# Performance work log

Measured on AMD Instinct MI355X. Metric: run time of the kernel, lower is better.

## Reference

```python
import jax, jax.numpy as jnp
import numpy as np

B, T, D, U = 32, 512, 1024, 1024
EPS = 1e-08


def setup_inputs() -> dict:
    key = jax.random.key(0)
    k1, k2, k3 = jax.random.split(key, 3)
    # scale weights for numerical sanity (glorot/orthogonal-ish magnitudes)
    kernel = jax.random.normal(k1, (D, 4 * U), dtype=jnp.float32) * (1.0 / np.sqrt(D))
    recurrent_kernel = jax.random.normal(k2, (U, 4 * U), dtype=jnp.float32) * (1.0 / np.sqrt(U))
    bias = jnp.zeros((4 * U,), dtype=jnp.float32)
    x = jax.random.normal(k3, (B, T, D), dtype=jnp.float32)
    return {"x": x, "kernel": kernel, "recurrent_kernel": recurrent_kernel, "bias": bias}


def reference(x, kernel, recurrent_kernel, bias):
    """sLSTM (xLSTM Sec 2.2) with sigmoid forget gate + log/exp/max stabilization,
    scanned over the time axis. Returns h of shape (B, T, U)."""
    U_ = bias.shape[0] // 4
    Bsz = x.shape[0]
    # precompute input projections for all timesteps: (T, B, 4U)
    x_proj = jnp.einsum('btd,dg->tbg', x, kernel) + bias

    def step(carry, xp_t):
        h, c, n, m = carry
        proj = xp_t + h @ recurrent_kernel          # (B, 4U)
        i_p, f_p, o_p, z_p = jnp.split(proj, 4, axis=-1)
        log_f = jnp.log(jax.nn.sigmoid(f_p) + EPS)
        m_t = jnp.maximum(m + log_f, i_p)
        i_t = jnp.exp(i_p - m_t)
        f_t = jnp.exp(m + log_f - m_t)
        o_t = jax.nn.sigmoid(o_p)
        z_t = jnp.tanh(z_p)
        c_t = f_t * c + i_t * z_t
        n_t = f_t * n + i_t
        h_t = o_t * (c_t / (n_t + EPS))
        return (h_t, c_t, n_t, m_t), h_t

    zeros = jnp.zeros((Bsz, U_), dtype=x.dtype)
    init = (zeros, zeros, zeros, zeros)
    _, hs = jax.lax.scan(step, init, x_proj)        # hs: (T, B, U)
    return jnp.transpose(hs, (1, 0, 2))             # (B, T, U)
```

## Files before the change

### kernel.cpp

```cpp
#include <hip/hip_runtime.h>

typedef unsigned short u16;
typedef short short8 __attribute__((ext_vector_type(8)));
typedef float f32x4 __attribute__((ext_vector_type(4)));
typedef unsigned int u32x4 __attribute__((ext_vector_type(4)));
typedef unsigned int u32x2 __attribute__((ext_vector_type(2)));
typedef unsigned short u16x4 __attribute__((ext_vector_type(4)));

#define Bsz 32
#define Tsz 512
#define Dsz 1024
#define Usz 1024
#define Gsz 4096

static __device__ __forceinline__ u16 f2bf(float f) {
    unsigned int u = __float_as_uint(f);
    unsigned int lsb = (u >> 16) & 1u;
    u += 0x7fffu + lsb;
    return (u16)(u >> 16);
}
static __device__ __forceinline__ float bf2f(u16 b) {
    return __uint_as_float(((unsigned int)b) << 16);
}


__global__ __launch_bounds__(256) void pack_a(const float* __restrict__ x, u16* __restrict__ Af) {
    size_t tid = (size_t)blockIdx.x * 256 + threadIdx.x;
    int L = (int)(tid & 63);
    size_t mtkb = tid >> 6;
    int kb = (int)(mtkb & 31);
    int mt = (int)(mtkb >> 5);
    int m  = mt * 16 + (L & 15);
    int d0 = kb * 32 + (L >> 4) * 8;
    const float* src = x + (size_t)m * Dsz + d0;
    short8 v;
#pragma unroll
    for (int j = 0; j < 8; ++j) v[j] = (short)f2bf(src[j]);
    *(short8*)(Af + tid * 8) = v;
}

__global__ __launch_bounds__(256) void pack_b(const float* __restrict__ W, u16* __restrict__ Bf) {
    size_t tid = (size_t)blockIdx.x * 256 + threadIdx.x;
    int L = (int)(tid & 63);
    size_t ntkb = tid >> 6;
    int kb = (int)(ntkb & 31);
    int nt = (int)(ntkb >> 5);
    int n  = nt * 16 + (L & 15);
    int k0 = kb * 32 + (L >> 4) * 8;
    short8 v;
#pragma unroll
    for (int j = 0; j < 8; ++j) v[j] = (short)f2bf(W[(size_t)(k0 + j) * Gsz + n]);
    *(short8*)(Bf + tid * 8) = v;
}

__global__ __launch_bounds__(256) void pack_r(const float* __restrict__ R, u16* __restrict__ Rp,
                                              unsigned* __restrict__ flags) {
    if (blockIdx.x < 2) flags[blockIdx.x * 256 + threadIdx.x] = 0;
    size_t tid = (size_t)blockIdx.x * 256 + threadIdx.x;
    int L = (int)(tid & 63);
    size_t bkkb = tid >> 6;
    int kb  = (int)(bkkb & 31);
    int blk = (int)(bkkb >> 5);
    int c = L & 15;
    int gate = c >> 2, du = c & 3;
    int g = gate * 1024 + blk * 4 + du;
    int k0 = kb * 32 + (L >> 4) * 8;
    short8 v;
#pragma unroll
    for (int j = 0; j < 8; ++j) v[j] = (short)f2bf(R[(size_t)(k0 + j) * Gsz + g]);
    *(short8*)(Rp + tid * 8) = v;
}

__global__ __launch_bounds__(256) void gemm1(const u16* __restrict__ Af, const u16* __restrict__ Bf,
                                             float* __restrict__ xpf, u16* __restrict__ xph, int xp32) {
    __shared__ u16 smem[16 * 512];
    int bm = blockIdx.x >> 5;
    int bn = blockIdx.x & 31;
    int tid = threadIdx.x;
    int w = tid >> 6, ln = tid & 63;
    int mw = w & 1, nw = w >> 1;

    f32x4 acc[4][4];
#pragma unroll
    for (int i = 0; i < 4; ++i)
#pragma unroll
        for (int j = 0; j < 4; ++j) acc[i][j] = (f32x4){0.f, 0.f, 0.f, 0.f};

    for (int kb = 0; kb < 32; ++kb) {
        short8 tmp[4];
#pragma unroll
        for (int c2 = 0; c2 < 4; ++c2) {
            int chunk = w * 4 + c2;
            const u16* src = (chunk < 8)
                ? Af + (((size_t)(bm * 8 + chunk) * 32 + kb) * 64 + ln) * 8
                : Bf + (((size_t)(bn * 8 + (chunk - 8)) * 32 + kb) * 64 + ln) * 8;
            tmp[c2] = *(const short8*)src;
        }
#pragma unroll
        for (int c2 = 0; c2 < 4; ++c2) {
            int chunk = w * 4 + c2;
            *(short8*)(smem + chunk * 512 + ln * 8) = tmp[c2];
        }
        __syncthreads();
        short8 av[4], bv[4];
#pragma unroll
        for (int i = 0; i < 4; ++i) av[i] = *(const short8*)(smem + (mw * 4 + i) * 512 + ln * 8);
#pragma unroll
        for (int j = 0; j < 4; ++j) bv[j] = *(const short8*)(smem + (8 + nw * 4 + j) * 512 + ln * 8);
#pragma unroll
        for (int i = 0; i < 4; ++i)
#pragma unroll
            for (int j = 0; j < 4; ++j)
                acc[i][j] = __builtin_amdgcn_mfma_f32_16x16x32_bf16(av[i], bv[j], acc[i][j], 0, 0, 0);
        __syncthreads();
    }

    int quad = ln >> 4, c15 = ln & 15;
#pragma unroll
    for (int i = 0; i < 4; ++i) {
        int mt_g = bm * 8 + mw * 4 + i;
#pragma unroll
        for (int j = 0; j < 4; ++j) {
            int g = (bn * 8 + nw * 4 + j) * 16 + c15;
            int p = ((g & 1023) >> 2) * 16 + (g & 3) * 4 + (g >> 10);
#pragma unroll
            for (int r = 0; r < 4; ++r) {
                int row = mt_g * 16 + quad * 4 + r;
                int bb = row >> 9, tt = row & 511;
                size_t o = ((size_t)tt * Bsz + bb) * Gsz + p;
                if (xp32) xpf[o] = acc[i][j][r];
                else      xph[o] = f2bf(acc[i][j][r]);
            }
        }
    }
}

__global__ __launch_bounds__(384) void scan_all(const float* __restrict__ xpf,
                                                const u16* __restrict__ xph, int xp32,
                                                const u16* __restrict__ Rp,
                                                const float* __restrict__ bias,
                                                u16* __restrict__ hbf, float* __restrict__ out,
                                                unsigned* __restrict__ flags) {
    __shared__ u16 lds_r[16384];
    __shared__ f32x4 partial[2][4][64];
    __shared__ float proj[16][17];

    int tid = threadIdx.x;
    int blk = blockIdx.x;
    int w = tid >> 6, ln = tid & 63, quad = ln >> 4, c15 = ln & 15;
    int bq = ln >> 2, du = ln & 3;
    int u_g = blk * 4 + du;

    unsigned* flags0 = flags;
    unsigned* flags1 = flags + 256;

    u16* h00 = hbf;
    u16* h01 = hbf + 16384;
    u16* h10 = hbf + 32768;
    u16* h11 = hbf + 49152;

    if (tid < 256) {
#pragma unroll
        for (int i = 0; i < 8; ++i)
            *(short8*)(lds_r + tid * 64 + i * 8) = *(const short8*)(Rp + (size_t)blk * 16384 + tid * 64 + i * 8);
        u32x4 z = (u32x4){0u, 0u, 0u, 0u};
#pragma unroll
        for (int i = 0; i < 8; ++i) {
            u16* p0 = h01 + tid * 64 + i * 8;
            u16* p1 = h11 + tid * 64 + i * 8;
            asm volatile("global_store_dwordx4 %0, %1, off sc0 sc1" :: "v"(p0), "v"(z) : "memory");
            asm volatile("global_store_dwordx4 %0, %1, off sc0 sc1" :: "v"(p1), "v"(z) : "memory");
        }
    }

    float bi0 = 0.f, bi1 = 0.f, bi2 = 0.f, bi3 = 0.f;
    float cs = 0.f, ns = 0.f, ms = 0.f;
    f32x4 xr4 = (f32x4){0.f, 0.f, 0.f, 0.f};
    u32x2 xr2 = (u32x2){0u, 0u};

    if (w >= 4) {
        int G = w - 4;
        bi0 = bias[u_g]; bi1 = bias[1024 + u_g]; bi2 = bias[2048 + u_g]; bi3 = bias[3072 + u_g];
        size_t o0 = (size_t)(G * 16 + bq) * Gsz + blk * 16 + du * 4;
        if (xp32) xr4 = *(const f32x4*)(xpf + o0);
        else      xr2 = *(const u32x2*)(xph + o0);
    }
    asm volatile("s_waitcnt vmcnt(0)" ::: "memory");
    __syncthreads();
    if (tid == 0) {
        unsigned one = 1;
        unsigned* f0 = flags0 + blk;
        unsigned* f1 = flags1 + blk;
        asm volatile("global_store_dword %0, %1, off sc0 sc1" :: "v"(f0), "v"(one) : "memory");
        asm volatile("global_store_dword %0, %1, off sc0 sc1" :: "v"(f1), "v"(one) : "memory");
    }

    auto phase = [&](int G, int t) {
        if (w < 4) {
            const unsigned* fp4 = (G ? flags1 : flags0) + ln * 4;
            unsigned tgt = (unsigned)(t + 1);
            u32x4 fv;
            do {
                asm volatile("global_load_dwordx4 %0, %1, off sc0 sc1\n\ts_waitcnt vmcnt(0)"
                             : "=v"(fv) : "v"(fp4) : "memory");
            } while (__any((int)(fv[0] < tgt || fv[1] < tgt || fv[2] < tgt || fv[3] < tgt)));

            const u16* hload = G ? ((t & 1) ? h10 : h11) : ((t & 1) ? h00 : h01);
            const u16* aBw = hload + (size_t)c15 * 1024 + w * 256 + quad * 8;
            short8 av[8];
#define LDH(i, OFF) asm volatile("global_load_dwordx4 %0, %1, off offset:" OFF " sc0 sc1" \
                                 : "=v"(av[i]) : "v"(aBw))
            LDH(0, "0");   LDH(1, "64");  LDH(2, "128"); LDH(3, "192");
            LDH(4, "256"); LDH(5, "320"); LDH(6, "384"); LDH(7, "448");
#undef LDH
            asm volatile("s_waitcnt vmcnt(0)" ::: "memory");
            __builtin_amdgcn_sched_barrier(0);

            f32x4 a0 = (f32x4){0.f, 0.f, 0.f, 0.f};
            f32x4 a1 = (f32x4){0.f, 0.f, 0.f, 0.f};
#pragma unroll
            for (int kk = 0; kk < 8; kk += 2) {
                short8 b0 = *(const short8*)(lds_r + ((w * 8 + kk) * 64 + ln) * 8);
                short8 b1 = *(const short8*)(lds_r + ((w * 8 + kk + 1) * 64 + ln) * 8);
                a0 = __builtin_amdgcn_mfma_f32_16x16x32_bf16(av[kk], b0, a0, 0, 0, 0);
                a1 = __builtin_amdgcn_mfma_f32_16x16x32_bf16(av[kk + 1], b1, a1, 0, 0, 0);
            }
            partial[G][w][ln] = a0 + a1;
        }
        __syncthreads();
        if (w == 4 + G) {
            f32x4 s = partial[G][0][ln];
            s += partial[G][1][ln];
            s += partial[G][2][ln];
            s += partial[G][3][ln];
#pragma unroll
            for (int r = 0; r < 4; ++r) proj[quad * 4 + r][c15] = s[r];
            asm volatile("s_waitcnt lgkmcnt(0)" ::: "memory");
            __builtin_amdgcn_sched_barrier(0);

            asm volatile("s_waitcnt vmcnt(0)" : "+v"(xr4), "+v"(xr2) :: "memory");
            __builtin_amdgcn_sched_barrier(0);
            float xv0, xv1, xv2, xv3;
            if (xp32) { xv0 = xr4[0]; xv1 = xr4[1]; xv2 = xr4[2]; xv3 = xr4[3]; }
            else {
                xv0 = bf2f((u16)(xr2[0] & 0xffffu)); xv1 = bf2f((u16)(xr2[0] >> 16));
                xv2 = bf2f((u16)(xr2[1] & 0xffffu)); xv3 = bf2f((u16)(xr2[1] >> 16));
            }

            float ip  = proj[bq][du]      + xv0 + bi0;
            float fp_ = proj[bq][4 + du]  + xv1 + bi1;
            float op_ = proj[bq][8 + du]  + xv2 + bi2;
            float zp  = proj[bq][12 + du] + xv3 + bi3;
            float sf = 1.f / (1.f + __expf(-fp_));
            float lf = __logf(sf + 1e-8f);
            float mn = fmaxf(ms + lf, ip);
            float it = __expf(ip - mn);
            float ft = __expf(ms + lf - mn);
            float ot = 1.f / (1.f + __expf(-op_));
            float zt = tanhf(zp);
            cs = ft * cs + it * zt;
            ns = ft * ns + it;
            ms = mn;
            float h = ot * (cs / (ns + 1e-8f));
            out[(size_t)(G * 16 + bq) * (Tsz * Usz) + (size_t)t * Usz + u_g] = h;
            u16* hstore = G ? ((t & 1) ? h11 : h10) : ((t & 1) ? h01 : h00);
            u16* hp = hstore + bq * 1024 + u_g;
            unsigned hv = (unsigned)f2bf(h);
            asm volatile("global_store_short %0, %1, off sc0 sc1" :: "v"(hp), "v"(hv) : "memory");
            asm volatile("s_waitcnt vmcnt(0)" ::: "memory");
            __builtin_amdgcn_sched_barrier(0);
            if (ln == 0) {
                unsigned* fm = (G ? flags1 : flags0) + blk;
                unsigned val = (unsigned)(t + 2);
                asm volatile("global_store_dword %0, %1, off sc0 sc1" :: "v"(fm), "v"(val) : "memory");
            }
            int tn = (t + 1 < Tsz) ? t + 1 : t;
            size_t o = ((size_t)tn * Bsz + (G * 16 + bq)) * Gsz + blk * 16 + du * 4;
            if (xp32) {
                const float* p = xpf + o;
                asm volatile("global_load_dwordx4 %0, %1, off" : "=v"(xr4) : "v"(p));
            } else {
                const u16* p = xph + o;
                asm volatile("global_load_dwordx2 %0, %1, off" : "=v"(xr2) : "v"(p));
            }
        }
    };

    for (int t = 0; t < Tsz; ++t) {
        phase(0, t);
        phase(1, t);
    }
}

extern "C" void kernel_launch(void* const* d_in, const int* in_sizes, int n_in,
                              void* d_out, int out_size, void* d_ws, size_t ws_size,
                              hipStream_t stream) {
    const float* x    = (const float*)d_in[0];
    const float* W    = (const float*)d_in[1];
    const float* R    = (const float*)d_in[2];
    const float* bias = (const float*)d_in[3];
    float* out = (float*)d_out;

    char* ws = (char*)d_ws;
    size_t off = 0;
    u16* Af = (u16*)(ws + off); off += (size_t)16384 * 1024 * 2;
    u16* Bf = (u16*)(ws + off); off += (size_t)1024 * 4096 * 2;
    u16* Rp = (u16*)(ws + off); off += (size_t)1024 * 4096 * 2;
    u16* hbf = (u16*)(ws + off); off += (size_t)1 << 20;
    unsigned* flags = (unsigned*)(ws + off); off += 4096;
    size_t xp_need32 = (size_t)16384 * 4096 * 4;
    int xp32 = (ws_size >= off + xp_need32) ? 1 : 0;
    float* xpf = (float*)(ws + off);
    u16*   xph = (u16*)(ws + off);

    pack_a<<<dim3(8192), dim3(256), 0, stream>>>(x, Af);
    pack_b<<<dim3(2048), dim3(256), 0, stream>>>(W, Bf);
    pack_r<<<dim3(2048), dim3(256), 0, stream>>>(R, Rp, flags);
    gemm1<<<dim3(4096), dim3(256), 0, stream>>>(Af, Bf, xpf, xph, xp32);

    void* args[] = { (void*)&xpf, (void*)&xph, (void*)&xp32, (void*)&Rp,
                     (void*)&bias, (void*)&hbf, (void*)&out, (void*)&flags };
    hipLaunchCooperativeKernel((const void*)scan_all, dim3(256), dim3(384), args, 0, stream);
}
```

Measured before the change: 2.615 ms.

## Specialize scan waves with LDS flag handoff instead of block barriers

Splits the persistent scan block into role-specialized waves: two poller waves spin on global flags and publish readiness through LDS, four MFMA waves keep their recurrent-weight slice in registers instead of LDS, and two gate waves consume double-buffered partials. Per-step __syncthreads are replaced by volatile LDS counters, so the two batch halves can pipeline independently. The block grows to 512 threads. This adds register pressure, spin-waiting on LDS, and a risk of memory-ordering bugs in the flag handoff.

Result: slower. 5.068 ms (+93.8%).

```diff
diff --git a/kernel.cpp b/kernel.cpp
--- a/kernel.cpp
+++ b/kernel.cpp
@@ -135,15 +135,16 @@
     }
 }
 
-__global__ __launch_bounds__(384) void scan_all(const float* __restrict__ xpf,
+__global__ __launch_bounds__(512) void scan_all(const float* __restrict__ xpf,
                                                 const u16* __restrict__ xph, int xp32,
                                                 const u16* __restrict__ Rp,
                                                 const float* __restrict__ bias,
                                                 u16* __restrict__ hbf, float* __restrict__ out,
                                                 unsigned* __restrict__ flags) {
-    __shared__ u16 lds_r[16384];
-    __shared__ f32x4 partial[2][4][64];
-    __shared__ float proj[16][17];
+    __shared__ f32x4 partial[2][2][4][64];
+    __shared__ float proj[2][16][17];
+    __shared__ int ready_sh[2];
+    __shared__ int done_sh[2][4];
 
     int tid = threadIdx.x;
     int blk = blockIdx.x;
@@ -159,10 +160,10 @@
     u16* h10 = hbf + 32768;
     u16* h11 = hbf + 49152;
 
+    if (tid == 0) { ready_sh[0] = 0; ready_sh[1] = 0; }
+    if (tid < 8) ((int*)done_sh)[tid] = 0;
+
     if (tid < 256) {
-#pragma unroll
-        for (int i = 0; i < 8; ++i)
-            *(short8*)(lds_r + tid * 64 + i * 8) = *(const short8*)(Rp + (size_t)blk * 16384 + tid * 64 + i * 8);
         u32x4 z = (u32x4){0u, 0u, 0u, 0u};
 #pragma unroll
         for (int i = 0; i < 8; ++i) {
@@ -174,11 +175,10 @@
     }
 
     float bi0 = 0.f, bi1 = 0.f, bi2 = 0.f, bi3 = 0.f;
-    float cs = 0.f, ns = 0.f, ms = 0.f;
     f32x4 xr4 = (f32x4){0.f, 0.f, 0.f, 0.f};
     u32x2 xr2 = (u32x2){0u, 0u};
 
-    if (w >= 4) {
+    if (w == 4 || w == 5) {
         int G = w - 4;
         bi0 = bias[u_g]; bi1 = bias[1024 + u_g]; bi2 = bias[2048 + u_g]; bi3 = bias[3072 + u_g];
         size_t o0 = (size_t)(G * 16 + bq) * Gsz + blk * 16 + du * 4;
@@ -186,6 +186,7 @@
         else      xr2 = *(const u32x2*)(xph + o0);
     }
     asm volatile("s_waitcnt vmcnt(0)" ::: "memory");
+    __builtin_amdgcn_sched_barrier(0);
     __syncthreads();
     if (tid == 0) {
         unsigned one = 1;
@@ -195,46 +196,61 @@
         asm volatile("global_store_dword %0, %1, off sc0 sc1" :: "v"(f1), "v"(one) : "memory");
     }
 
-    auto phase = [&](int G, int t) {
-        if (w < 4) {
-            const unsigned* fp4 = (G ? flags1 : flags0) + ln * 4;
-            unsigned tgt = (unsigned)(t + 1);
-            u32x4 fv;
-            do {
-                asm volatile("global_load_dwordx4 %0, %1, off sc0 sc1\n\ts_waitcnt vmcnt(0)"
-                             : "=v"(fv) : "v"(fp4) : "memory");
-            } while (__any((int)(fv[0] < tgt || fv[1] < tgt || fv[2] < tgt || fv[3] < tgt)));
-
-            const u16* hload = G ? ((t & 1) ? h10 : h11) : ((t & 1) ? h00 : h01);
-            const u16* aBw = hload + (size_t)c15 * 1024 + w * 256 + quad * 8;
-            short8 av[8];
+    if (w < 4) {
+        short8 rB[8];
+#pragma unroll
+        for (int kk = 0; kk < 8; ++kk)
+            rB[kk] = *(const short8*)(Rp + (size_t)blk * 16384 + (size_t)(((w * 8 + kk) * 64 + ln) * 8));
+
+        volatile int* rdy0 = &ready_sh[0];
+        volatile int* rdy1 = &ready_sh[1];
+
+        for (int t = 0; t < Tsz; ++t) {
+#pragma unroll
+            for (int G = 0; G < 2; ++G) {
+                volatile int* rdy = G ? rdy1 : rdy0;
+                while (*rdy < t + 1) { }
+                __builtin_amdgcn_sched_barrier(0);
+
+                const u16* hload = G ? ((t & 1) ? h10 : h11) : ((t & 1) ? h00 : h01);
+                const u16* aBw = hload + (size_t)c15 * 1024 + w * 256 + quad * 8;
+                short8 av[8];
 #define LDH(i, OFF) asm volatile("global_load_dwordx4 %0, %1, off offset:" OFF " sc0 sc1" \
                                  : "=v"(av[i]) : "v"(aBw))
-            LDH(0, "0");   LDH(1, "64");  LDH(2, "128"); LDH(3, "192");
-            LDH(4, "256"); LDH(5, "320"); LDH(6, "384"); LDH(7, "448");
+                LDH(0, "0");   LDH(1, "64");  LDH(2, "128"); LDH(3, "192");
+                LDH(4, "256"); LDH(5, "320"); LDH(6, "384"); LDH(7, "448");
 #undef LDH
-            asm volatile("s_waitcnt vmcnt(0)" ::: "memory");
-            __builtin_amdgcn_sched_barrier(0);
-
-            f32x4 a0 = (f32x4){0.f, 0.f, 0.f, 0.f};
-            f32x4 a1 = (f32x4){0.f, 0.f, 0.f, 0.f};
-#pragma unroll
-            for (int kk = 0; kk < 8; kk += 2) {
-                short8 b0 = *(const short8*)(lds_r + ((w * 8 + kk) * 64 + ln) * 8);
-                short8 b1 = *(const short8*)(lds_r + ((w * 8 + kk + 1) * 64 + ln) * 8);
-                a0 = __builtin_amdgcn_mfma_f32_16x16x32_bf16(av[kk], b0, a0, 0, 0, 0);
-                a1 = __builtin_amdgcn_mfma_f32_16x16x32_bf16(av[kk + 1], b1, a1, 0, 0, 0);
-            }
-            partial[G][w][ln] = a0 + a1;
-        }
-        __syncthreads();
-        if (w == 4 + G) {
-            f32x4 s = partial[G][0][ln];
-            s += partial[G][1][ln];
-            s += partial[G][2][ln];
-            s += partial[G][3][ln];
-#pragma unroll
-            for (int r = 0; r < 4; ++r) proj[quad * 4 + r][c15] = s[r];
+                asm volatile("s_waitcnt vmcnt(0)" ::: "memory");
+                __builtin_amdgcn_sched_barrier(0);
+
+                f32x4 a0 = (f32x4){0.f, 0.f, 0.f, 0.f};
+                f32x4 a1 = (f32x4){0.f, 0.f, 0.f, 0.f};
+#pragma unroll
+                for (int kk = 0; kk < 8; kk += 2) {
+                    a0 = __builtin_amdgcn_mfma_f32_16x16x32_bf16(av[kk],     rB[kk],     a0, 0, 0, 0);
+                    a1 = __builtin_amdgcn_mfma_f32_16x16x32_bf16(av[kk + 1], rB[kk + 1], a1, 0, 0, 0);
+                }
+                partial[G][t & 1][w][ln] = a0 + a1;
+                asm volatile("s_waitcnt lgkmcnt(0)" ::: "memory");
+                __builtin_amdgcn_sched_barrier(0);
+                if (ln == 0) *((volatile int*)&done_sh[G][w]) = t + 1;
+            }
+        }
+    } else if (w < 6) {
+        int G = w - 4;
+        float cs = 0.f, ns = 0.f, ms = 0.f;
+        volatile int* dp = &done_sh[G][ln & 3];
+
+        for (int t = 0; t < Tsz; ++t) {
+            while (__any(*dp < t + 1)) { }
+            __builtin_amdgcn_sched_barrier(0);
+
+            f32x4 s = partial[G][t & 1][0][ln];
+            s += partial[G][t & 1][1][ln];
+            s += partial[G][t & 1][2][ln];
+            s += partial[G][t & 1][3][ln];
+#pragma unroll
+            for (int r = 0; r < 4; ++r) proj[G][quad * 4 + r][c15] = s[r];
             asm volatile("s_waitcnt lgkmcnt(0)" ::: "memory");
             __builtin_amdgcn_sched_barrier(0);
 
@@ -247,10 +263,10 @@
                 xv2 = bf2f((u16)(xr2[1] & 0xffffu)); xv3 = bf2f((u16)(xr2[1] >> 16));
             }
 
-            float ip  = proj[bq][du]      + xv0 + bi0;
-            float fp_ = proj[bq][4 + du]  + xv1 + bi1;
-            float op_ = proj[bq][8 + du]  + xv2 + bi2;
-            float zp  = proj[bq][12 + du] + xv3 + bi3;
+            float ip  = proj[G][bq][du]      + xv0 + bi0;
+            float fp_ = proj[G][bq][4 + du]  + xv1 + bi1;
+            float op_ = proj[G][bq][8 + du]  + xv2 + bi2;
+            float zp  = proj[G][bq][12 + du] + xv3 + bi3;
             float sf = 1.f / (1.f + __expf(-fp_));
             float lf = __logf(sf + 1e-8f);
             float mn = fmaxf(ms + lf, ip);
@@ -284,11 +300,19 @@
                 asm volatile("global_load_dwordx2 %0, %1, off" : "=v"(xr2) : "v"(p));
             }
         }
-    };
-
-    for (int t = 0; t < Tsz; ++t) {
-        phase(0, t);
-        phase(1, t);
+    } else {
+        int G = w - 6;
+        const unsigned* fp4 = (G ? flags1 : flags0) + ln * 4;
+        for (int s = 1; s <= Tsz; ++s) {
+            unsigned tgt = (unsigned)s;
+            u32x4 fv;
+            do {
+                asm volatile("global_load_dwordx4 %0, %1, off sc0 sc1\n\ts_waitcnt vmcnt(0)"
+                             : "=v"(fv) : "v"(fp4) : "memory");
+            } while (__any((int)(fv[0] < tgt || fv[1] < tgt || fv[2] < tgt || fv[3] < tgt)));
+            __builtin_amdgcn_sched_barrier(0);
+            if (ln == 0) *((volatile int*)&ready_sh[G]) = s;
+        }
     }
 }
 
@@ -320,5 +344,5 @@
 
     void* args[] = { (void*)&xpf, (void*)&xph, (void*)&xp32, (void*)&Rp,
                      (void*)&bias, (void*)&hbf, (void*)&out, (void*)&flags };
-    hipLaunchCooperativeKernel((const void*)scan_all, dim3(256), dim3(384), args, 0, stream);
-}
+    hipLaunchCooperativeKernel((const void*)scan_all, dim3(256), dim3(512), args, 0, stream);
+}
```

## Replace per-block flag polling with NaN-sentinel validity check on h buffers

Applied to the files above, without the earlier changes.

Removes the separate flag array and its spin loop. Consumers now load h directly and retry until no element holds the NaN sentinel. The h state becomes a 4-slot ring per group: each step writes h into one slot and resets the slot two steps ahead to the sentinel. pack_r initialises the ring instead of zeroing flags. This cuts the flag-poll round trip from the critical path of every timestep, at the risk of a false match if a real bf16 h value is NaN or Inf, plus extra sentinel stores and per-element checks.

Measured after the change: 2.472 ms. 1.06x faster.

```diff
diff --git a/kernel.cpp b/kernel.cpp
--- a/kernel.cpp
+++ b/kernel.cpp
@@ -5,13 +5,14 @@
 typedef float f32x4 __attribute__((ext_vector_type(4)));
 typedef unsigned int u32x4 __attribute__((ext_vector_type(4)));
 typedef unsigned int u32x2 __attribute__((ext_vector_type(2)));
-typedef unsigned short u16x4 __attribute__((ext_vector_type(4)));
 
 #define Bsz 32
 #define Tsz 512
 #define Dsz 1024
 #define Usz 1024
 #define Gsz 4096
+
+#define SENTINEL 0x7FC0u
 
 static __device__ __forceinline__ u16 f2bf(float f) {
     unsigned int u = __float_as_uint(f);
@@ -54,9 +55,12 @@
 }
 
 __global__ __launch_bounds__(256) void pack_r(const float* __restrict__ R, u16* __restrict__ Rp,
-                                              unsigned* __restrict__ flags) {
-    if (blockIdx.x < 2) flags[blockIdx.x * 256 + threadIdx.x] = 0;
+                                              u16* __restrict__ hbf) {
     size_t tid = (size_t)blockIdx.x * 256 + threadIdx.x;
+    if (tid < 131072) {
+        int p = (int)((tid >> 14) & 3);
+        hbf[tid] = (p == 3) ? (u16)0 : (u16)SENTINEL;
+    }
     int L = (int)(tid & 63);
     size_t bkkb = tid >> 6;
     int kb  = (int)(bkkb & 31);
@@ -139,11 +143,10 @@
                                                 const u16* __restrict__ xph, int xp32,
                                                 const u16* __restrict__ Rp,
                                                 const float* __restrict__ bias,
-                                                u16* __restrict__ hbf, float* __restrict__ out,
-                                                unsigned* __restrict__ flags) {
+                                                u16* __restrict__ hbf, float* __restrict__ out) {
     __shared__ u16 lds_r[16384];
     __shared__ f32x4 partial[2][4][64];
-    __shared__ float proj[16][17];
+    __shared__ float proj[2][16][17];
 
     int tid = threadIdx.x;
     int blk = blockIdx.x;
@@ -151,26 +154,10 @@
     int bq = ln >> 2, du = ln & 3;
     int u_g = blk * 4 + du;
 
-    unsigned* flags0 = flags;
-    unsigned* flags1 = flags + 256;
-
-    u16* h00 = hbf;
-    u16* h01 = hbf + 16384;
-    u16* h10 = hbf + 32768;
-    u16* h11 = hbf + 49152;
-
     if (tid < 256) {
 #pragma unroll
         for (int i = 0; i < 8; ++i)
             *(short8*)(lds_r + tid * 64 + i * 8) = *(const short8*)(Rp + (size_t)blk * 16384 + tid * 64 + i * 8);
-        u32x4 z = (u32x4){0u, 0u, 0u, 0u};
-#pragma unroll
-        for (int i = 0; i < 8; ++i) {
-            u16* p0 = h01 + tid * 64 + i * 8;
-            u16* p1 = h11 + tid * 64 + i * 8;
-            asm volatile("global_store_dwordx4 %0, %1, off sc0 sc1" :: "v"(p0), "v"(z) : "memory");
-            asm volatile("global_store_dwordx4 %0, %1, off sc0 sc1" :: "v"(p1), "v"(z) : "memory");
-        }
     }
 
     float bi0 = 0.f, bi1 = 0.f, bi2 = 0.f, bi3 = 0.f;
@@ -185,35 +172,35 @@
         if (xp32) xr4 = *(const f32x4*)(xpf + o0);
         else      xr2 = *(const u32x2*)(xph + o0);
     }
-    asm volatile("s_waitcnt vmcnt(0)" ::: "memory");
     __syncthreads();
-    if (tid == 0) {
-        unsigned one = 1;
-        unsigned* f0 = flags0 + blk;
-        unsigned* f1 = flags1 + blk;
-        asm volatile("global_store_dword %0, %1, off sc0 sc1" :: "v"(f0), "v"(one) : "memory");
-        asm volatile("global_store_dword %0, %1, off sc0 sc1" :: "v"(f1), "v"(one) : "memory");
-    }
 
     auto phase = [&](int G, int t) {
         if (w < 4) {
-            const unsigned* fp4 = (G ? flags1 : flags0) + ln * 4;
-            unsigned tgt = (unsigned)(t + 1);
-            u32x4 fv;
-            do {
-                asm volatile("global_load_dwordx4 %0, %1, off sc0 sc1\n\ts_waitcnt vmcnt(0)"
-                             : "=v"(fv) : "v"(fp4) : "memory");
-            } while (__any((int)(fv[0] < tgt || fv[1] < tgt || fv[2] < tgt || fv[3] < tgt)));
-
-            const u16* hload = G ? ((t & 1) ? h10 : h11) : ((t & 1) ? h00 : h01);
-            const u16* aBw = hload + (size_t)c15 * 1024 + w * 256 + quad * 8;
+            const u16* hbase = hbf + ((size_t)(G * 4 + ((t + 3) & 3)) << 14)
+                                   + (size_t)c15 * 1024 + w * 256 + quad * 8;
             short8 av[8];
+            for (;;) {
 #define LDH(i, OFF) asm volatile("global_load_dwordx4 %0, %1, off offset:" OFF " sc0 sc1" \
-                                 : "=v"(av[i]) : "v"(aBw))
-            LDH(0, "0");   LDH(1, "64");  LDH(2, "128"); LDH(3, "192");
-            LDH(4, "256"); LDH(5, "320"); LDH(6, "384"); LDH(7, "448");
+                                 : "=v"(av[i]) : "v"(hbase))
+                LDH(0, "0");   LDH(1, "64");  LDH(2, "128"); LDH(3, "192");
+                LDH(4, "256"); LDH(5, "320"); LDH(6, "384"); LDH(7, "448");
 #undef LDH
-            asm volatile("s_waitcnt vmcnt(0)" ::: "memory");
+                asm volatile("s_waitcnt vmcnt(0)" ::: "memory");
+                __builtin_amdgcn_sched_barrier(0);
+                unsigned bad = 0;
+#pragma unroll
+                for (int i = 0; i < 8; ++i) {
+                    u32x4 xw = __builtin_bit_cast(u32x4, av[i]);
+#pragma unroll
+                    for (int k = 0; k < 4; ++k) {
+                        unsigned m = xw[k] & 0x7F807F80u;
+                        bad |= (unsigned)((m >> 16) == 0x7F80u);
+                        bad |= (unsigned)((m & 0xFFFFu) == 0x7F80u);
+                    }
+                }
+                if (!__any((int)bad)) break;
+                asm volatile("s_sleep 1" ::: "memory");
+            }
             __builtin_amdgcn_sched_barrier(0);
 
             f32x4 a0 = (f32x4){0.f, 0.f, 0.f, 0.f};
@@ -234,7 +221,7 @@
             s += partial[G][2][ln];
             s += partial[G][3][ln];
 #pragma unroll
-            for (int r = 0; r < 4; ++r) proj[quad * 4 + r][c15] = s[r];
+            for (int r = 0; r < 4; ++r) proj[G][quad * 4 + r][c15] = s[r];
             asm volatile("s_waitcnt lgkmcnt(0)" ::: "memory");
             __builtin_amdgcn_sched_barrier(0);
 
@@ -247,10 +234,10 @@
                 xv2 = bf2f((u16)(xr2[1] & 0xffffu)); xv3 = bf2f((u16)(xr2[1] >> 16));
             }
 
-            float ip  = proj[bq][du]      + xv0 + bi0;
-            float fp_ = proj[bq][4 + du]  + xv1 + bi1;
-            float op_ = proj[bq][8 + du]  + xv2 + bi2;
-            float zp  = proj[bq][12 + du] + xv3 + bi3;
+            float ip  = proj[G][bq][du]      + xv0 + bi0;
+            float fp_ = proj[G][bq][4 + du]  + xv1 + bi1;
+            float op_ = proj[G][bq][8 + du]  + xv2 + bi2;
+            float zp  = proj[G][bq][12 + du] + xv3 + bi3;
             float sf = 1.f / (1.f + __expf(-fp_));
             float lf = __logf(sf + 1e-8f);
             float mn = fmaxf(ms + lf, ip);
@@ -263,17 +250,17 @@
             ms = mn;
             float h = ot * (cs / (ns + 1e-8f));
             out[(size_t)(G * 16 + bq) * (Tsz * Usz) + (size_t)t * Usz + u_g] = h;
-            u16* hstore = G ? ((t & 1) ? h11 : h10) : ((t & 1) ? h01 : h00);
-            u16* hp = hstore + bq * 1024 + u_g;
+
+            size_t chunk = (size_t)bq * 1024 + u_g;
+            u16* hp = hbf + ((size_t)(G * 4 + (t & 3)) << 14) + chunk;
+            u16* sp = hbf + ((size_t)(G * 4 + ((t + 2) & 3)) << 14) + chunk;
             unsigned hv = (unsigned)f2bf(h);
+            unsigned sv = SENTINEL;
             asm volatile("global_store_short %0, %1, off sc0 sc1" :: "v"(hp), "v"(hv) : "memory");
+            asm volatile("global_store_short %0, %1, off sc0 sc1" :: "v"(sp), "v"(sv) : "memory");
             asm volatile("s_waitcnt vmcnt(0)" ::: "memory");
             __builtin_amdgcn_sched_barrier(0);
-            if (ln == 0) {
-                unsigned* fm = (G ? flags1 : flags0) + blk;
-                unsigned val = (unsigned)(t + 2);
-                asm volatile("global_store_dword %0, %1, off sc0 sc1" :: "v"(fm), "v"(val) : "memory");
-            }
+
             int tn = (t + 1 < Tsz) ? t + 1 : t;
             size_t o = ((size_t)tn * Bsz + (G * 16 + bq)) * Gsz + blk * 16 + du * 4;
             if (xp32) {
@@ -307,7 +294,7 @@
     u16* Bf = (u16*)(ws + off); off += (size_t)1024 * 4096 * 2;
     u16* Rp = (u16*)(ws + off); off += (size_t)1024 * 4096 * 2;
     u16* hbf = (u16*)(ws + off); off += (size_t)1 << 20;
-    unsigned* flags = (unsigned*)(ws + off); off += 4096;
+    off += 4096;
     size_t xp_need32 = (size_t)16384 * 4096 * 4;
     int xp32 = (ws_size >= off + xp_need32) ? 1 : 0;
     float* xpf = (float*)(ws + off);
@@ -315,10 +302,10 @@
 
     pack_a<<<dim3(8192), dim3(256), 0, stream>>>(x, Af);
     pack_b<<<dim3(2048), dim3(256), 0, stream>>>(W, Bf);
-    pack_r<<<dim3(2048), dim3(256), 0, stream>>>(R, Rp, flags);
+    pack_r<<<dim3(2048), dim3(256), 0, stream>>>(R, Rp, hbf);
     gemm1<<<dim3(4096), dim3(256), 0, stream>>>(Af, Bf, xpf, xph, xp32);
 
     void* args[] = { (void*)&xpf, (void*)&xph, (void*)&xp32, (void*)&Rp,
-                     (void*)&bias, (void*)&hbf, (void*)&out, (void*)&flags };
+                     (void*)&bias, (void*)&hbf, (void*)&out };
     hipLaunchCooperativeKernel((const void*)scan_all, dim3(256), dim3(384), args, 0, stream);
 }
```
